# Performance work log

Hardware: AMD Instinct MI355X
Metric: run time of the kernel (lower is better)

Reference implementation:

```python
import jax, jax.numpy as jnp
import numpy as np

H = 8  # n_heads

def setup_inputs() -> dict:
    key = jax.random.key(0)
    k1, k2, k3, k4, k5 = jax.random.split(key, 5)
    B, N, D = 4, 2048, 512
    x = jax.random.normal(k1, (B, N, D), dtype=jnp.float32)
    mask_flat = jax.random.randint(k2, (B, N), 0, 2).astype(bool)
    s = 1.0 / np.sqrt(D)
    Wq = jax.random.normal(k3, (D, D), dtype=jnp.float32) * s
    Wkv = jax.random.normal(k4, (D, 2 * D), dtype=jnp.float32) * s
    Wo = jax.random.normal(k5, (D, D), dtype=jnp.float32) * s
    return {"x": x, "mask_flat": mask_flat, "Wq": Wq, "Wkv": Wkv, "Wo": Wo}

def reference(x, mask_flat, Wq, Wkv, Wo):
    B, N, D = x.shape
    d = D // H
    scale = d ** -0.5
    kv = x @ Wkv                                   # (B,N,2D)
    k, v = jnp.split(kv, 2, axis=-1)
    q = x @ Wq                                     # (B,N,D)
    # (B,H,N,d)
    q = q.reshape(B, N, H, d).transpose(0, 2, 1, 3)
    k = k.reshape(B, N, H, d).transpose(0, 2, 1, 3)
    v = v.reshape(B, N, H, d).transpose(0, 2, 1, 3)
    attn = jax.nn.softmax(jnp.einsum('bhmd,bhnd->bhmn', q, k) * scale, axis=-1)
    res = jnp.einsum('bhmn,bhnd->bhmd', attn, v)   # (B,H,N,d)
    out = res.transpose(0, 2, 1, 3).reshape(B, N, D) @ Wo
    # non-masked query positions produce zero output (residual elsewhere keeps them)
    return jnp.where(mask_flat[..., None], out, 0.0)
```

## Files before the change

### kernel.cpp

```cpp
#include <hip/hip_runtime.h>

typedef __bf16 bf16x8 __attribute__((ext_vector_type(8)));
typedef float f32x4 __attribute__((ext_vector_type(4)));
typedef float f32x16 __attribute__((ext_vector_type(16)));
typedef unsigned short u16x8 __attribute__((ext_vector_type(8)));
typedef unsigned int u32x4 __attribute__((ext_vector_type(4)));
typedef int i32x2 __attribute__((ext_vector_type(2)));

__device__ inline unsigned short f2bf(float f) {
    __bf16 h = (__bf16)f;
    return __builtin_bit_cast(unsigned short, h);
}

__device__ inline unsigned int pkbf(float lo, float hi) {
    return (unsigned int)f2bf(lo) | ((unsigned int)f2bf(hi) << 16);
}

__device__ inline float fexp2(float x) {
#if __has_builtin(__builtin_amdgcn_exp2f)
    return __builtin_amdgcn_exp2f(x);
#else
    return exp2f(x);
#endif
}

__device__ inline f32x4 mfma16(u16x8 a, u16x8 b, f32x4 c) {
    return __builtin_amdgcn_mfma_f32_16x16x32_bf16(
        __builtin_bit_cast(bf16x8, a), __builtin_bit_cast(bf16x8, b), c, 0, 0, 0);
}

__device__ inline f32x16 mfma32(u16x8 a, u16x8 b, f32x16 c) {
    return __builtin_amdgcn_mfma_f32_32x32x16_bf16(
        __builtin_bit_cast(bf16x8, a), __builtin_bit_cast(bf16x8, b), c, 0, 0, 0);
}

__device__ inline i32x2 permswap(unsigned int a, unsigned int b, int hi) {
#if __has_builtin(__builtin_amdgcn_permlane32_swap)
    (void)hi;
    return __builtin_amdgcn_permlane32_swap((int)a, (int)b, false, false);
#else
    int pa_ = __shfl_xor((int)a, 32);
    int pb_ = __shfl_xor((int)b, 32);
    i32x2 r;
    r[0] = hi ? pb_ : (int)a;
    r[1] = hi ? (int)b : pa_;
    return r;
#endif
}

__device__ inline void gld_lds16(const unsigned short* gsrc, unsigned short* ldst) {
    __builtin_amdgcn_global_load_lds(
        (const __attribute__((address_space(1))) unsigned int*)gsrc,
        (__attribute__((address_space(3))) unsigned int*)ldst, 16, 0, 0);
}

#define WAIT_VM(n)                                          \
    asm volatile("s_waitcnt vmcnt(" #n ")" ::: "memory");   \
    __builtin_amdgcn_sched_barrier(0)
#define WAIT_LGKM0                                          \
    asm volatile("s_waitcnt lgkmcnt(0)" ::: "memory");      \
    __builtin_amdgcn_sched_barrier(0)
#define BARRIER                                             \
    __builtin_amdgcn_s_barrier();                           \
    __builtin_amdgcn_sched_barrier(0)

__global__ __launch_bounds__(256) void cvt_f32_bf16(const float* __restrict__ in,
                                                    unsigned short* __restrict__ out, long n) {
    long i = ((long)blockIdx.x * blockDim.x + threadIdx.x) * 4;
    if (i >= n) return;
    float4 v = *(const float4*)(in + i);
    ushort4 r;
    r.x = f2bf(v.x); r.y = f2bf(v.y); r.z = f2bf(v.z); r.w = f2bf(v.w);
    *(ushort4*)(out + i) = r;
}

__global__ __launch_bounds__(256) void prep_weights(const float* __restrict__ Wq,
                                                    const float* __restrict__ Wkv,
                                                    const float* __restrict__ Wo,
                                                    unsigned short* __restrict__ WqkvT,
                                                    unsigned short* __restrict__ WoT,
                                                    float qscale) {
    __shared__ float tile[64][65];
    const int z = blockIdx.z;
    if (z != 1 && blockIdx.x >= 8) return;
    const float* W = (z == 0) ? Wq : (z == 1) ? Wkv : Wo;
    unsigned short* Wt = (z == 0) ? WqkvT : (z == 1) ? (WqkvT + 512L * 512) : WoT;
    const int N = (z == 1) ? 1024 : 512;
    const float scale = (z == 0) ? qscale : 1.0f;
    const int K = 512;
    const int n0 = blockIdx.x * 64, k0 = blockIdx.y * 64;
    const int c = threadIdx.x & 63;
    const int r4 = threadIdx.x >> 6;
#pragma unroll
    for (int i = 0; i < 16; i++) {
        int r = r4 * 16 + i;
        tile[r][c] = W[(long)(k0 + r) * N + n0 + c];
    }
    __syncthreads();
#pragma unroll
    for (int i = 0; i < 16; i++) {
        int rr = r4 * 16 + i;
        Wt[(long)(n0 + rr) * K + k0 + c] = f2bf(tile[c][rr] * scale);
    }
}

__global__ __launch_bounds__(256) void scan_mask(const int* __restrict__ mask,
                                                 int* __restrict__ idx, int* __restrict__ cnt) {
    const int b = blockIdx.x;
    const int tid = threadIdx.x;
    __shared__ int wsum[4];
    int m[8]; int pc = 0;
#pragma unroll
    for (int k = 0; k < 8; k++) { m[k] = mask[b * 2048 + tid * 8 + k]; pc += (m[k] != 0); }
    int s = pc;
    const int lane = tid & 63;
    for (int off = 1; off < 64; off <<= 1) {
        int v = __shfl_up(s, off);
        if (lane >= off) s += v;
    }
    if (lane == 63) wsum[tid >> 6] = s;
    __syncthreads();
    int wbase = 0;
    for (int w = 0; w < (tid >> 6); w++) wbase += wsum[w];
    int run = wbase + s - pc;
#pragma unroll
    for (int k = 0; k < 8; k++) if (m[k]) idx[b * 2048 + (run++)] = tid * 8 + k;
    if (tid == 255) cnt[b] = wbase + s;
}

template<int WRITE_BF16, int MASKED>
__global__ __launch_bounds__(256) void gemm_bt(const unsigned short* __restrict__ A,
                                               const unsigned short* __restrict__ Bt,
                                               void* __restrict__ Cv,
                                               int M, int N, int K,
                                               const int* __restrict__ mask) {
    __shared__ unsigned short AsL[2][128 * 32];
    __shared__ unsigned short BsL[2][128 * 32];
    const int tid = threadIdx.x;
    const int lane = tid & 63;
    const int wid = tid >> 6;
    const int lg = lane >> 4, lr = lane & 15;
    const int wm = wid >> 1, wn = wid & 1;
    const long m0 = (long)blockIdx.y * 128, n0 = (long)blockIdx.x * 128;

    f32x4 acc[4][4] = {};

    const unsigned short* aS0 = A  + (m0 + (tid >> 2)) * K + (tid & 3) * 8;
    const unsigned short* aS1 = A  + (m0 + 64 + (tid >> 2)) * K + (tid & 3) * 8;
    const unsigned short* bS0 = Bt + (n0 + (tid >> 2)) * K + (tid & 3) * 8;
    const unsigned short* bS1 = Bt + (n0 + 64 + (tid >> 2)) * K + (tid & 3) * 8;

#define GSTAGE(bufi, k0v)                                    \
    {                                                        \
        gld_lds16(aS0 + (k0v), &AsL[bufi][wid * 512]);       \
        gld_lds16(aS1 + (k0v), &AsL[bufi][2048 + wid * 512]);\
        gld_lds16(bS0 + (k0v), &BsL[bufi][wid * 512]);       \
        gld_lds16(bS1 + (k0v), &BsL[bufi][2048 + wid * 512]);\
    }
#define GREAD(cur)                                                                    \
    {                                                                                 \
        _Pragma("unroll")                                                             \
        for (int i = 0; i < 4; i++) {                                                 \
            af[i]  = *(const u16x8*)&AsL[cur][(wm * 64 + i * 16 + lr) * 32 + lg * 8]; \
            bfr[i] = *(const u16x8*)&BsL[cur][(wn * 64 + i * 16 + lr) * 32 + lg * 8]; \
        }                                                                             \
    }
#define GMFMA                                                                  \
    {                                                                          \
        _Pragma("unroll")                                                      \
        for (int i = 0; i < 4; i++)                                            \
            _Pragma("unroll")                                                  \
            for (int j = 0; j < 4; j++)                                        \
                acc[i][j] = mfma16(af[i], bfr[j], acc[i][j]);                  \
    }

    const int nk = K >> 5;
    GSTAGE(0, 0);
    GSTAGE(1, 32);
    for (int t = 0; t < nk - 1; t++) {
        const int cur = t & 1;
        u16x8 af[4], bfr[4];
        WAIT_VM(4);
        BARRIER;
        GREAD(cur);
        WAIT_LGKM0;
        BARRIER;
        if (t < nk - 2) GSTAGE(cur, (t + 2) * 32);
        GMFMA;
    }
    {
        u16x8 af[4], bfr[4];
        WAIT_VM(0);
        BARRIER;
        GREAD((nk - 1) & 1);
        GMFMA;
    }
#undef GSTAGE
#undef GREAD
#undef GMFMA

#pragma unroll
    for (int i = 0; i < 4; i++)
#pragma unroll
        for (int j = 0; j < 4; j++)
#pragma unroll
            for (int r = 0; r < 4; r++) {
                long row = m0 + wm * 64 + i * 16 + lg * 4 + r;
                long col = n0 + wn * 64 + j * 16 + lr;
                float v = acc[i][j][r];
                if (MASKED) {
                    if (!mask[row]) v = 0.0f;
                    ((float*)Cv)[row * N + col] = v;
                } else if (WRITE_BF16) {
                    ((unsigned short*)Cv)[row * N + col] = f2bf(v);
                } else {
                    ((float*)Cv)[row * N + col] = v;
                }
            }
}

__global__ __launch_bounds__(128) void attn_kernel(const unsigned short* __restrict__ qk,
                                                   const unsigned short* __restrict__ vT,
                                                   unsigned short* __restrict__ res,
                                                   const int* __restrict__ idxm,
                                                   const int* __restrict__ cntm) {
    const int Nseq = 2048, LD = 1024;
    const long T = 8192;
    const int id = blockIdx.x;
    const int xcd = id & 7, jj = id >> 3;
    const int g = xcd + 8 * (jj & 3);
    const int qt = jj >> 2;
    const int b = g >> 3, h = g & 7;

    const int count = cntm[b];
    if (qt * 32 >= count) return;

    const int tid = threadIdx.x;
    const int wid = tid >> 6, lane = tid & 63;
    const int qL = lane & 31, hi = lane >> 5;
    const int kvh = wid;

    __shared__ unsigned short LDSB[2][2][4096];
    unsigned short* myL = &LDSB[kvh][0][0];

    const int i_q = qt * 32 + qL;
    const int gi = idxm[b * 2048 + (i_q < count ? i_q : count - 1)];
    const long qrow = (long)b * Nseq + gi;
    u16x8 qf[4];
#pragma unroll
    for (int j = 0; j < 4; j++)
        qf[j] = *(const u16x8*)(qk + qrow * LD + h * 64 + 16 * j + 8 * hi);

    f32x16 oacc[2] = {};
    f32x16 lacc = {};
    u16x8 onesf;
#pragma unroll
    for (int e = 0; e < 8; e++) onesf[e] = 0x3F80;

    const int R0 = lane >> 3, p0 = lane & 7;
    const unsigned short* kS = qk + 512 + ((long)b * Nseq + kvh * 1024 + R0) * LD + h * 64
                               + ((p0 ^ R0) * 8);
    const int rV = lane >> 2, pV = lane & 3;
    const unsigned short* vS = vT + ((long)h * 64 + rV) * T + (long)b * Nseq + kvh * 1024
                               + ((pV ^ ((lane >> 3) & 3)) * 8);
    const int rsw = qL & 7;

#define STAGE(bufi)                                                          \
    {                                                                        \
        unsigned short* dK = myL + (bufi) * 4096;                            \
        _Pragma("unroll")                                                    \
        for (int i = 0; i < 4; i++)                                          \
            gld_lds16(kS + (long)i * 8 * LD, dK + i * 512);                  \
        _Pragma("unroll")                                                    \
        for (int i = 0; i < 4; i++)                                          \
            gld_lds16(vS + (long)i * 16 * T, dK + 2048 + i * 512);           \
        kS += 32L * LD; vS += 32;                                            \
    }

#define READ_KF(buf)                                                           \
    {                                                                          \
        _Pragma("unroll")                                                      \
        for (int j = 0; j < 4; j++)                                            \
            kf[j] = *(const u16x8*)&myL[(buf) * 4096 + qL * 64                 \
                                        + (((2 * j + hi) ^ rsw) * 8)];         \
    }
#define READ_VF(buf)                                                           \
    {                                                                          \
        _Pragma("unroll")                                                      \
        for (int db = 0; db < 2; db++)                                         \
            _Pragma("unroll")                                                  \
            for (int jk = 0; jk < 2; jk++)                                     \
                vf[db][jk] = *(const u16x8*)&myL[(buf) * 4096 + 2048           \
                                 + (db * 32 + qL) * 32                         \
                                 + (((2 * jk + hi) ^ ((qL >> 1) & 3)) * 8)];   \
    }

#define QKNEXT(SN)                                                             \
    {                                                                          \
        SN = (f32x16){};                                                       \
        _Pragma("unroll")                                                      \
        for (int j = 0; j < 4; j++) SN = mfma32(kf[j], qf[j], SN);             \
    }

#define PACK_PV(SC)                                                                    \
    {                                                                                  \
        unsigned int w[8];                                                             \
        _Pragma("unroll")                                                              \
        for (int i = 0; i < 8; i++)                                                    \
            w[i] = pkbf(fexp2(SC[2 * i]), fexp2(SC[2 * i + 1]));                       \
        u16x8 pa[2];                                                                   \
        _Pragma("unroll")                                                              \
        for (int hh = 0; hh < 2; hh++) {                                               \
            i32x2 ra = permswap(w[4 * hh + 0], w[4 * hh + 2], hi);                     \
            i32x2 rb = permswap(w[4 * hh + 1], w[4 * hh + 3], hi);                     \
            u32x4 fw;                                                                  \
            fw[0] = (unsigned)ra[0]; fw[1] = (unsigned)rb[0];                          \
            fw[2] = (unsigned)ra[1]; fw[3] = (unsigned)rb[1];                          \
            pa[hh] = __builtin_bit_cast(u16x8, fw);                                    \
        }                                                                              \
        _Pragma("unroll")                                                              \
        for (int jk = 0; jk < 2; jk++) {                                               \
            lacc = mfma32(pa[jk], onesf, lacc);                                        \
            oacc[0] = mfma32(pa[jk], vf[0][jk], oacc[0]);                              \
            oacc[1] = mfma32(pa[jk], vf[1][jk], oacc[1]);                              \
        }                                                                              \
    }

#define STEP(SC, SN, cur)                                                      \
    {                                                                          \
        WAIT_VM(4);                                                            \
        READ_VF(cur);                                                          \
        READ_KF(cur ^ 1);                                                      \
        WAIT_LGKM0;                                                            \
        STAGE(cur);                                                            \
        QKNEXT(SN);                                                            \
        PACK_PV(SC);                                                           \
    }

    u16x8 kf[4], vf[2][2];
    f32x16 sA, sB;

    STAGE(0);
    STAGE(1);
    WAIT_VM(12);
    READ_KF(0);
    WAIT_LGKM0;
    QKNEXT(sA);

    for (int t = 0; t < 30; t += 2) {
        STEP(sA, sB, 0);
        STEP(sB, sA, 1);
    }
    {
        WAIT_VM(4);
        READ_VF(0);
        READ_KF(1);
        WAIT_LGKM0;
        QKNEXT(sB);
        PACK_PV(sA);
    }
    {
        WAIT_VM(0);
        READ_VF(1);
        WAIT_LGKM0;
        PACK_PV(sB);
    }
#undef STAGE
#undef READ_KF
#undef READ_VF
#undef QKNEXT
#undef PACK_PV
#undef STEP

    __syncthreads();
    float* Ox = (float*)&LDSB[0][0][0];
    float* lX = Ox + 32 * 65;

    if (kvh == 1) {
#pragma unroll
        for (int reg = 0; reg < 16; reg++) {
            const int crow = (reg & 3) + 8 * (reg >> 2) + 4 * hi;
            Ox[crow * 65 + qL]      = oacc[0][reg];
            Ox[crow * 65 + 32 + qL] = oacc[1][reg];
            lX[crow] = lacc[reg];
        }
    }
    __syncthreads();
    if (kvh == 0) {
#pragma unroll
        for (int reg = 0; reg < 16; reg++) {
            const int crow = (reg & 3) + 8 * (reg >> 2) + 4 * hi;
            const int row_c = qt * 32 + crow;
            if (row_c < count) {
                float lt = lacc[reg] + lX[crow];
                float linv = 1.0f / lt;
                float o0 = oacc[0][reg] + Ox[crow * 65 + qL];
                float o1 = oacc[1][reg] + Ox[crow * 65 + 32 + qL];
                const int orig = idxm[b * 2048 + row_c];
                long row = (long)b * Nseq + orig;
                res[row * 512 + h * 64 + qL]      = f2bf(o0 * linv);
                res[row * 512 + h * 64 + 32 + qL] = f2bf(o1 * linv);
            }
        }
    }
}

extern "C" void kernel_launch(void* const* d_in, const int* in_sizes, int n_in,
                              void* d_out, int out_size, void* d_ws, size_t ws_size,
                              hipStream_t stream) {
    const float* x   = (const float*)d_in[0];
    const int* mask  = (const int*)d_in[1];
    const float* Wq  = (const float*)d_in[2];
    const float* Wkv = (const float*)d_in[3];
    const float* Wo  = (const float*)d_in[4];
    float* out = (float*)d_out;

    const int Nseq = 2048, D = 512;
    const long T = 8192;
    const float QSCALE = 0.125f * 1.4426950408889634f;

    unsigned short* ws    = (unsigned short*)d_ws;
    unsigned short* xb    = ws;
    unsigned short* WqkvT = xb    + T * D;
    unsigned short* WoT   = WqkvT + 1536L * 512;
    unsigned short* qkb   = WoT   + 512L * 512;
    unsigned short* vTb   = qkb   + T * 1024;
    unsigned short* resb  = vTb   + 512L * T;
    int* idxb = (int*)(resb + T * 512);
    int* cntb = idxb + 4 * 2048;

    cvt_f32_bf16<<<(int)(T * D / 1024), 256, 0, stream>>>(x, xb, T * D);
    prep_weights<<<dim3(16, 8, 3), 256, 0, stream>>>(Wq, Wkv, Wo, WqkvT, WoT, QSCALE);
    scan_mask<<<4, 256, 0, stream>>>(mask, idxb, cntb);

    gemm_bt<1, 0><<<dim3(8, 64), 256, 0, stream>>>(xb, WqkvT, qkb, T, 1024, D, nullptr);
    gemm_bt<1, 0><<<dim3(64, 4), 256, 0, stream>>>(WqkvT + 1024L * 512, xb, vTb, D, T, D, nullptr);

    attn_kernel<<<2048, 128, 0, stream>>>(qkb, vTb, resb, idxb, cntb);

    gemm_bt<0, 1><<<dim3(4, 64), 256, 0, stream>>>(resb, WoT, out, T, D, D, mask);
}
```

Baseline: 101.8 us.

## Fuse QKV projections into one GEMM and widen attention blocks to 8 waves

Replaces the two separate projection GEMMs (QK and transposed V) with a single gemm_qkv launch that writes Q/K row-major and V transposed, using vectorized 4-element stores for the V part. The attention kernel now uses 512-thread blocks that handle 64 queries with the KV sequence split four ways. Pairs of query waves share the K/V tiles in LDS, synchronized with barriers. Partial outputs from the four KV splits are combined through LDS at the end. This cuts launch count and duplicate K/V loads, but adds block-wide barriers in the inner loop and a larger cross-wave reduction.

```diff
diff --git a/kernel.cpp b/kernel.cpp
--- a/kernel.cpp
+++ b/kernel.cpp
@@ -4,6 +4,7 @@
 typedef float f32x4 __attribute__((ext_vector_type(4)));
 typedef float f32x16 __attribute__((ext_vector_type(16)));
 typedef unsigned short u16x8 __attribute__((ext_vector_type(8)));
+typedef unsigned short u16x4 __attribute__((ext_vector_type(4)));
 typedef unsigned int u32x4 __attribute__((ext_vector_type(4)));
 typedef int i32x2 __attribute__((ext_vector_type(2)));
 
@@ -128,6 +129,102 @@
     if (tid == 255) cnt[b] = wbase + s;
 }
 
+__global__ __launch_bounds__(256) void gemm_qkv(const unsigned short* __restrict__ A,
+                                                const unsigned short* __restrict__ Bt,
+                                                unsigned short* __restrict__ qkb,
+                                                unsigned short* __restrict__ vT) {
+    const int K = 512;
+    __shared__ unsigned short AsL[2][128 * 32];
+    __shared__ unsigned short BsL[2][128 * 32];
+    const int tid = threadIdx.x;
+    const int lane = tid & 63;
+    const int wid = tid >> 6;
+    const int lg = lane >> 4, lr = lane & 15;
+    const int wm = wid >> 1, wn = wid & 1;
+    const long m0 = (long)blockIdx.y * 128, n0 = (long)blockIdx.x * 128;
+
+    f32x4 acc[4][4] = {};
+
+    const unsigned short* aS0 = A  + (m0 + (tid >> 2)) * K + (tid & 3) * 8;
+    const unsigned short* aS1 = A  + (m0 + 64 + (tid >> 2)) * K + (tid & 3) * 8;
+    const unsigned short* bS0 = Bt + (n0 + (tid >> 2)) * K + (tid & 3) * 8;
+    const unsigned short* bS1 = Bt + (n0 + 64 + (tid >> 2)) * K + (tid & 3) * 8;
+
+#define GSTAGE(bufi, k0v)                                    \
+    {                                                        \
+        gld_lds16(aS0 + (k0v), &AsL[bufi][wid * 512]);       \
+        gld_lds16(aS1 + (k0v), &AsL[bufi][2048 + wid * 512]);\
+        gld_lds16(bS0 + (k0v), &BsL[bufi][wid * 512]);       \
+        gld_lds16(bS1 + (k0v), &BsL[bufi][2048 + wid * 512]);\
+    }
+#define GREAD(cur)                                                                    \
+    {                                                                                 \
+        _Pragma("unroll")                                                             \
+        for (int i = 0; i < 4; i++) {                                                 \
+            af[i]  = *(const u16x8*)&AsL[cur][(wm * 64 + i * 16 + lr) * 32 + lg * 8]; \
+            bfr[i] = *(const u16x8*)&BsL[cur][(wn * 64 + i * 16 + lr) * 32 + lg * 8]; \
+        }                                                                             \
+    }
+#define GMFMA                                                                  \
+    {                                                                          \
+        _Pragma("unroll")                                                      \
+        for (int i = 0; i < 4; i++)                                            \
+            _Pragma("unroll")                                                  \
+            for (int j = 0; j < 4; j++)                                        \
+                acc[i][j] = mfma16(af[i], bfr[j], acc[i][j]);                  \
+    }
+
+    const int nk = K >> 5;
+    GSTAGE(0, 0);
+    GSTAGE(1, 32);
+    for (int t = 0; t < nk - 1; t++) {
+        const int cur = t & 1;
+        u16x8 af[4], bfr[4];
+        WAIT_VM(4);
+        BARRIER;
+        GREAD(cur);
+        WAIT_LGKM0;
+        BARRIER;
+        if (t < nk - 2) GSTAGE(cur, (t + 2) * 32);
+        GMFMA;
+    }
+    {
+        u16x8 af[4], bfr[4];
+        WAIT_VM(0);
+        BARRIER;
+        GREAD((nk - 1) & 1);
+        GMFMA;
+    }
+#undef GSTAGE
+#undef GREAD
+#undef GMFMA
+
+    if (n0 < 1024) {
+#pragma unroll
+        for (int i = 0; i < 4; i++)
+#pragma unroll
+            for (int j = 0; j < 4; j++)
+#pragma unroll
+                for (int r = 0; r < 4; r++) {
+                    long row = m0 + wm * 64 + i * 16 + lg * 4 + r;
+                    long col = n0 + wn * 64 + j * 16 + lr;
+                    qkb[row * 1024 + col] = f2bf(acc[i][j][r]);
+                }
+    } else {
+#pragma unroll
+        for (int i = 0; i < 4; i++)
+#pragma unroll
+            for (int j = 0; j < 4; j++) {
+                long vd = n0 - 1024 + wn * 64 + j * 16 + lr;
+                long tok0 = m0 + wm * 64 + i * 16 + lg * 4;
+                u16x4 st;
+#pragma unroll
+                for (int r = 0; r < 4; r++) st[r] = f2bf(acc[i][j][r]);
+                *(u16x4*)&vT[vd * 8192 + tok0] = st;
+            }
+    }
+}
+
 template<int WRITE_BF16, int MASKED>
 __global__ __launch_bounds__(256) void gemm_bt(const unsigned short* __restrict__ A,
                                                const unsigned short* __restrict__ Bt,
@@ -219,11 +316,11 @@
             }
 }
 
-__global__ __launch_bounds__(128) void attn_kernel(const unsigned short* __restrict__ qk,
-                                                   const unsigned short* __restrict__ vT,
-                                                   unsigned short* __restrict__ res,
-                                                   const int* __restrict__ idxm,
-                                                   const int* __restrict__ cntm) {
+__global__ __launch_bounds__(512, 4) void attn_kernel(const unsigned short* __restrict__ qk,
+                                                      const unsigned short* __restrict__ vT,
+                                                      unsigned short* __restrict__ res,
+                                                      const int* __restrict__ idxm,
+                                                      const int* __restrict__ cntm) {
     const int Nseq = 2048, LD = 1024;
     const long T = 8192;
     const int id = blockIdx.x;
@@ -233,17 +330,16 @@
     const int b = g >> 3, h = g & 7;
 
     const int count = cntm[b];
-    if (qt * 32 >= count) return;
+    if (qt * 64 >= count) return;
 
     const int tid = threadIdx.x;
     const int wid = tid >> 6, lane = tid & 63;
     const int qL = lane & 31, hi = lane >> 5;
-    const int kvh = wid;
-
-    __shared__ unsigned short LDSB[2][2][4096];
-    unsigned short* myL = &LDSB[kvh][0][0];
-
-    const int i_q = qt * 32 + qL;
+    const int qh = wid >> 2, kvq = wid & 3;
+
+    __shared__ unsigned short LDSB[4][2][4096];
+
+    const int i_q = qt * 64 + qh * 32 + qL;
     const int gi = idxm[b * 2048 + (i_q < count ? i_q : count - 1)];
     const long qrow = (long)b * Nseq + gi;
     u16x8 qf[4];
@@ -257,49 +353,49 @@
 #pragma unroll
     for (int e = 0; e < 8; e++) onesf[e] = 0x3F80;
 
-    const int R0 = lane >> 3, p0 = lane & 7;
-    const unsigned short* kS = qk + 512 + ((long)b * Nseq + kvh * 1024 + R0) * LD + h * 64
-                               + ((p0 ^ R0) * 8);
+    const int Rs = lane >> 3, p0 = lane & 7;
+    const unsigned short* kS = qk + 512
+        + ((long)b * Nseq + kvq * 512 + qh * 16 + Rs) * LD + h * 64 + ((p0 ^ Rs) * 8);
     const int rV = lane >> 2, pV = lane & 3;
-    const unsigned short* vS = vT + ((long)h * 64 + rV) * T + (long)b * Nseq + kvh * 1024
-                               + ((pV ^ ((lane >> 3) & 3)) * 8);
+    const unsigned short* vS = vT + ((long)h * 64 + qh * 32 + rV) * T
+        + (long)b * Nseq + kvq * 512 + ((pV ^ ((lane >> 3) & 3)) * 8);
     const int rsw = qL & 7;
 
-#define STAGE(bufi)                                                          \
-    {                                                                        \
-        unsigned short* dK = myL + (bufi) * 4096;                            \
-        _Pragma("unroll")                                                    \
-        for (int i = 0; i < 4; i++)                                          \
-            gld_lds16(kS + (long)i * 8 * LD, dK + i * 512);                  \
-        _Pragma("unroll")                                                    \
-        for (int i = 0; i < 4; i++)                                          \
-            gld_lds16(vS + (long)i * 16 * T, dK + 2048 + i * 512);           \
-        kS += 32L * LD; vS += 32;                                            \
-    }
-
-#define READ_KF(buf)                                                           \
-    {                                                                          \
-        _Pragma("unroll")                                                      \
-        for (int j = 0; j < 4; j++)                                            \
-            kf[j] = *(const u16x8*)&myL[(buf) * 4096 + qL * 64                 \
-                                        + (((2 * j + hi) ^ rsw) * 8)];         \
-    }
-#define READ_VF(buf)                                                           \
-    {                                                                          \
-        _Pragma("unroll")                                                      \
-        for (int db = 0; db < 2; db++)                                         \
-            _Pragma("unroll")                                                  \
-            for (int jk = 0; jk < 2; jk++)                                     \
-                vf[db][jk] = *(const u16x8*)&myL[(buf) * 4096 + 2048           \
-                                 + (db * 32 + qL) * 32                         \
-                                 + (((2 * jk + hi) ^ ((qL >> 1) & 3)) * 8)];   \
-    }
-
-#define QKNEXT(SN)                                                             \
-    {                                                                          \
-        SN = (f32x16){};                                                       \
-        _Pragma("unroll")                                                      \
-        for (int j = 0; j < 4; j++) SN = mfma32(kf[j], qf[j], SN);             \
+#define STAGE(bufi)                                                              \
+    {                                                                            \
+        unsigned short* dK = &LDSB[kvq][bufi][0];                                \
+        _Pragma("unroll")                                                        \
+        for (int i = 0; i < 2; i++)                                              \
+            gld_lds16(kS + (long)i * 8 * LD, dK + qh * 1024 + i * 512);          \
+        _Pragma("unroll")                                                        \
+        for (int i = 0; i < 2; i++)                                              \
+            gld_lds16(vS + (long)i * 16 * T, dK + 2048 + qh * 1024 + i * 512);   \
+        kS += 32L * LD; vS += 32;                                                \
+    }
+
+#define READ_KF(buf)                                                             \
+    {                                                                            \
+        _Pragma("unroll")                                                        \
+        for (int j = 0; j < 4; j++)                                              \
+            kf[j] = *(const u16x8*)&LDSB[kvq][buf][qL * 64                       \
+                                        + (((2 * j + hi) ^ rsw) * 8)];           \
+    }
+#define READ_VF(buf)                                                             \
+    {                                                                            \
+        _Pragma("unroll")                                                        \
+        for (int db = 0; db < 2; db++)                                           \
+            _Pragma("unroll")                                                    \
+            for (int jk = 0; jk < 2; jk++)                                       \
+                vf[db][jk] = *(const u16x8*)&LDSB[kvq][buf][2048                 \
+                                 + (db * 32 + qL) * 32                           \
+                                 + (((2 * jk + hi) ^ ((qL >> 1) & 3)) * 8)];     \
+    }
+
+#define QKNEXT(SN)                                                               \
+    {                                                                            \
+        SN = (f32x16){};                                                         \
+        _Pragma("unroll")                                                        \
+        for (int j = 0; j < 4; j++) SN = mfma32(kf[j], qf[j], SN);               \
     }
 
 #define PACK_PV(SC)                                                                    \
@@ -326,15 +422,17 @@
         }                                                                              \
     }
 
-#define STEP(SC, SN, cur)                                                      \
-    {                                                                          \
-        WAIT_VM(4);                                                            \
-        READ_VF(cur);                                                          \
-        READ_KF(cur ^ 1);                                                      \
-        WAIT_LGKM0;                                                            \
-        STAGE(cur);                                                            \
-        QKNEXT(SN);                                                            \
-        PACK_PV(SC);                                                           \
+#define STEP(SC, SN, cur)                                                        \
+    {                                                                            \
+        WAIT_VM(2);                \
+        BARRIER;                                              \
+        READ_VF(cur);                                                            \
+        READ_KF(cur ^ 1);                                                        \
+        WAIT_LGKM0;                                                              \
+        BARRIER;                 \
+        STAGE(cur);                                                              \
+        QKNEXT(SN);                                                              \
+        PACK_PV(SC);                                                             \
     }
 
     u16x8 kf[4], vf[2][2];
@@ -342,17 +440,19 @@
 
     STAGE(0);
     STAGE(1);
-    WAIT_VM(12);
+    WAIT_VM(6);
+    BARRIER;
     READ_KF(0);
     WAIT_LGKM0;
     QKNEXT(sA);
 
-    for (int t = 0; t < 30; t += 2) {
+    for (int t = 0; t < 14; t += 2) {
         STEP(sA, sB, 0);
         STEP(sB, sA, 1);
     }
     {
-        WAIT_VM(4);
+        WAIT_VM(2);
+        BARRIER;
         READ_VF(0);
         READ_KF(1);
         WAIT_LGKM0;
@@ -361,6 +461,7 @@
     }
     {
         WAIT_VM(0);
+        BARRIER;
         READ_VF(1);
         WAIT_LGKM0;
         PACK_PV(sB);
@@ -374,28 +475,35 @@
 
     __syncthreads();
     float* Ox = (float*)&LDSB[0][0][0];
-    float* lX = Ox + 32 * 65;
-
-    if (kvh == 1) {
+    float* lX = Ox + 3 * 2 * 2080;
+
+    if (kvq != 0) {
+        const int set = kvq - 1;
 #pragma unroll
         for (int reg = 0; reg < 16; reg++) {
             const int crow = (reg & 3) + 8 * (reg >> 2) + 4 * hi;
-            Ox[crow * 65 + qL]      = oacc[0][reg];
-            Ox[crow * 65 + 32 + qL] = oacc[1][reg];
-            lX[crow] = lacc[reg];
+            Ox[(set * 2 + qh) * 2080 + crow * 65 + qL]      = oacc[0][reg];
+            Ox[(set * 2 + qh) * 2080 + crow * 65 + 32 + qL] = oacc[1][reg];
+            lX[(set * 2 + qh) * 32 + crow] = lacc[reg];
         }
     }
     __syncthreads();
-    if (kvh == 0) {
+    if (kvq == 0) {
 #pragma unroll
         for (int reg = 0; reg < 16; reg++) {
             const int crow = (reg & 3) + 8 * (reg >> 2) + 4 * hi;
-            const int row_c = qt * 32 + crow;
+            const int row_c = qt * 64 + qh * 32 + crow;
             if (row_c < count) {
-                float lt = lacc[reg] + lX[crow];
+                float lt = lacc[reg];
+                float o0 = oacc[0][reg];
+                float o1 = oacc[1][reg];
+#pragma unroll
+                for (int set = 0; set < 3; set++) {
+                    lt += lX[(set * 2 + qh) * 32 + crow];
+                    o0 += Ox[(set * 2 + qh) * 2080 + crow * 65 + qL];
+                    o1 += Ox[(set * 2 + qh) * 2080 + crow * 65 + 32 + qL];
+                }
                 float linv = 1.0f / lt;
-                float o0 = oacc[0][reg] + Ox[crow * 65 + qL];
-                float o1 = oacc[1][reg] + Ox[crow * 65 + 32 + qL];
                 const int orig = idxm[b * 2048 + row_c];
                 long row = (long)b * Nseq + orig;
                 res[row * 512 + h * 64 + qL]      = f2bf(o0 * linv);
@@ -433,10 +541,9 @@
     prep_weights<<<dim3(16, 8, 3), 256, 0, stream>>>(Wq, Wkv, Wo, WqkvT, WoT, QSCALE);
     scan_mask<<<4, 256, 0, stream>>>(mask, idxb, cntb);
 
-    gemm_bt<1, 0><<<dim3(8, 64), 256, 0, stream>>>(xb, WqkvT, qkb, T, 1024, D, nullptr);
-    gemm_bt<1, 0><<<dim3(64, 4), 256, 0, stream>>>(WqkvT + 1024L * 512, xb, vTb, D, T, D, nullptr);
-
-    attn_kernel<<<2048, 128, 0, stream>>>(qkb, vTb, resb, idxb, cntb);
+    gemm_qkv<<<dim3(12, 64), 256, 0, stream>>>(xb, WqkvT, qkb, vTb);
+
+    attn_kernel<<<1024, 512, 0, stream>>>(qkb, vTb, resb, idxb, cntb);
 
     gemm_bt<0, 1><<<dim3(4, 64), 256, 0, stream>>>(resb, WoT, out, T, D, D, mask);
 }
```

Result: slower. 139.1 us (+36.6%).
